# Kernel optimization log

Hardware: AMD Instinct MI355X
Metric: run time of the kernel (lower is better)

The kernel has to match this reference:

```python
import jax, jax.numpy as jnp
import numpy as np

K = 4  # correlation radius -> (2K+1)**2 = 81 displacement channels


def setup_inputs() -> dict:
    key = jax.random.key(0)
    kx, ky = jax.random.split(key)
    x = jax.random.normal(kx, (4, 64, 256, 256), dtype=jnp.float32)
    y = jax.random.normal(ky, (4, 64, 256, 256), dtype=jnp.float32)
    return {"x": x, "y": y}


def reference(x, y):
    b, c, ph, pw = x.shape
    k = K
    # reflect-pad y by k on both spatial dims (matches F.pad(..., 'reflect'))
    yp = jnp.pad(y, ((0, 0), (0, 0), (k, k), (k, k)), mode="reflect")
    # fixed 81-offset loop (trace-time); each term: channel-sum correlation
    outs = [
        jnp.sum(x * jax.lax.dynamic_slice(yp, (0, 0, k + i, k + j), (b, c, ph, pw)), axis=1)
        for i in range(-k, k + 1)
        for j in range(-k, k + 1)
    ]
    return jnp.stack(outs, axis=1)  # [b, (2k+1)^2, ph, pw]
```

## Files before the change

kernel.cpp:

```cpp
#include <hip/hip_runtime.h>


#define HH   256
#define WW   256
#define CCH  64
#define KRAD 4
#define ND   81

#define WT   16
#define HT   16
#define WY   24
#define RSTRIDE 128
#define YRING 10
#define YSLOT (WY * RSTRIDE)
#define PSTRIDE 68

typedef __attribute__((ext_vector_type(8))) short bf16x8;
typedef __attribute__((ext_vector_type(4))) float f32x4;

__device__ __forceinline__ int reflect(int v, int n) {
    v = v < 0 ? -v : v;
    return v >= n ? 2 * n - 2 - v : v;
}
__device__ __forceinline__ unsigned f2bf_pk(float a, float b) {
    union { float f; unsigned u; } xa, xb;
    xa.f = a; xb.f = b;
    unsigned ra = (xa.u + 0x7fffu + ((xa.u >> 16) & 1u)) >> 16;
    unsigned rb = (xb.u + 0x7fffu + ((xb.u >> 16) & 1u)) >> 16;
    return ra | (rb << 16);
}
__device__ __forceinline__ int mod10(int s) {
    if (s >= 20) s -= 20; else if (s >= 10) s -= 10;
    return s;
}

__global__ __launch_bounds__(256, 4) void corr_mfma_kernel(
    const float* __restrict__ x, const float* __restrict__ y,
    float* __restrict__ out)
{
    __shared__ char lds[YRING * YSLOT + ND * PSTRIDE + 12];
    char* ylds   = lds;
    char* pstage = lds + YRING * YSLOT;

    const int d  = blockIdx.x;
    const int v  = (d & 7) * 128 + (d >> 3);
    const int b  = v >> 8;
    const int by = (v >> 4) & 15;
    const int bx = v & 15;
    const int w0 = bx * WT;
    const int h0 = by * HT;

    const int t    = threadIdx.x;
    const int wid  = t >> 6;
    const int lane = t & 63;
    const int lq   = lane >> 4;
    const int ln   = lane & 15;

    const size_t plane = (size_t)HH * WW;
    const float* yb = y + (size_t)b * CCH * plane;
    const float* xb = x + (size_t)b * CCH * plane;

    const int yp  = t & 31;
    const int ycg = t >> 5;

    auto loadY = [&](int hrow, float* v8) {
        int gh = reflect(hrow, HH);
        int pc = yp < WY ? yp : WY - 1;
        int gw = reflect(w0 - KRAD + pc, WW);
        const float* src = yb + (size_t)(ycg * 8) * plane + (size_t)gh * WW + gw;
#pragma unroll
        for (int j = 0; j < 8; ++j) v8[j] = src[(size_t)j * plane];
    };
    auto writeY = [&](int slot, const float* v8) {
        if (yp < WY) {
            char* dst = ylds + slot * YSLOT + yp * RSTRIDE
                      + (((unsigned)(ycg * 16)) ^ ((unsigned)(yp & 7) << 4));
            union { unsigned u[4]; uint4 q; } pk;
#pragma unroll
            for (int m = 0; m < 4; ++m)
                pk.u[m] = f2bf_pk(v8[2 * m], v8[2 * m + 1]);
            *(uint4*)dst = pk.q;
        }
    };
    auto loadX = [&](int hrow, float* v16) {
        int gh = reflect(hrow, HH);
        const float* src = xb + (size_t)(lq * 8) * plane + (size_t)gh * WW + (w0 + ln);
#pragma unroll
        for (int j = 0; j < 8; ++j) v16[j] = src[(size_t)j * plane];
        const float* src2 = src + (size_t)32 * plane;
#pragma unroll
        for (int j = 0; j < 8; ++j) v16[8 + j] = src2[(size_t)j * plane];
    };
    auto xconv = [&](const float* v16, bf16x8& f0, bf16x8& f1) {
        union { unsigned u[4]; bf16x8 v; } c0, c1;
#pragma unroll
        for (int m = 0; m < 4; ++m) {
            c0.u[m] = f2bf_pk(v16[2 * m], v16[2 * m + 1]);
            c1.u[m] = f2bf_pk(v16[8 + 2 * m], v16[9 + 2 * m]);
        }
        f0 = c0.v; f1 = c1.v;
    };

    float yv[8], yv2[8], xv[16];
    bf16x8 bf0, bf1;

    loadY(h0 - KRAD, yv);
    loadX(h0, xv);
#pragma unroll 1
    for (int j = 0; j < 9; ++j) {
        if (j < 8) loadY(h0 - KRAD + j + 1, yv2);
        writeY(j, yv);
#pragma unroll
        for (int m = 0; m < 8; ++m) yv[m] = yv2[m];
    }
    xconv(xv, bf0, bf1);
    __syncthreads();

    const int mbase = lq * 4;
    const int prow  = t >> 4;
    const int pcol  = t & 15;

#pragma unroll 1
    for (int hh = 0; hh < HT; ++hh) {
        const int h = h0 + hh;

        loadY(h + KRAD + 1, yv);
        loadX(h + 1, xv);

        for (int u = wid; u < 18; u += 4) {
            const int di = u >> 1;
            const int wt = u & 1;
            const int slot = mod10(hh + di);
            const char* abase = ylds + slot * YSLOT + (wt * 16 + ln) * RSTRIDE;
            const unsigned sw = (unsigned)(ln & 7) << 4;
            bf16x8 af0 = *(const bf16x8*)(abase + (((unsigned)(lq * 16)) ^ sw));
            bf16x8 af1 = *(const bf16x8*)(abase + (((unsigned)(64 + lq * 16)) ^ sw));
            f32x4 dacc = {0.f, 0.f, 0.f, 0.f};
            dacc = __builtin_amdgcn_mfma_f32_16x16x32_bf16(af0, bf0, dacc, 0, 0, 0);
            dacc = __builtin_amdgcn_mfma_f32_16x16x32_bf16(af1, bf1, dacc, 0, 0, 0);
            char* psu = pstage + di * (9 * PSTRIDE) + ln * 4;
#pragma unroll
            for (int r = 0; r < 4; ++r) {
                const int vr = mbase + r - ln + (wt ? 16 : 0);
                if ((unsigned)vr <= 8u)
                    *(float*)(psu + vr * PSTRIDE) = dacc[r];
            }
        }

        writeY(mod10(hh + 9), yv);
        xconv(xv, bf0, bf1);

        __builtin_amdgcn_sched_barrier(0);
        asm volatile("s_waitcnt lgkmcnt(0)" ::: "memory");
        __builtin_amdgcn_s_barrier();
        __builtin_amdgcn_sched_barrier(0);

        {
            float* og = out + (size_t)b * ND * plane + (size_t)h * WW + (w0 + pcol);
#pragma unroll
            for (int p = 0; p < 6; ++p) {
                const int didx = p * 16 + prow;
                if (p < 5 || prow == 0) {
                    float vv = *(const float*)(pstage + didx * PSTRIDE + pcol * 4);
                    og[(size_t)didx * plane] = vv;
                }
            }
        }

        __builtin_amdgcn_sched_barrier(0);
        __builtin_amdgcn_s_barrier();
        __builtin_amdgcn_sched_barrier(0);
    }
}

extern "C" void kernel_launch(void* const* d_in, const int* in_sizes, int n_in,
                              void* d_out, int out_size, void* d_ws, size_t ws_size,
                              hipStream_t stream) {
    const float* x = (const float*)d_in[0];
    const float* y = (const float*)d_in[1];
    float* out = (float*)d_out;

    dim3 grid(1024);
    dim3 block(256);
    corr_mfma_kernel<<<grid, block, 0, stream>>>(x, y, out);
}
```

Before: 57.59 us.

## Widen tile to 32 columns with 512-thread blocks and per-wave displacement split

Doubles the block tile width from 16 to 32 pixels and the block size to 512 threads, halving the grid. Each wave now owns a fixed 16x16 quadrant and a fixed range of vertical displacements, with the valid-store masks precomputed outside the loop. The wider tile cuts the share of the y halo that is reloaded, since 40 columns are loaded for 32 outputs instead of 24 for 16. In exchange it uses more LDS per block, leaves some threads idle during y loads, and adds an extra LDS wait before the second barrier.

```diff
diff --git a/kernel.cpp b/kernel.cpp
--- a/kernel.cpp
+++ b/kernel.cpp
@@ -7,13 +7,13 @@
 #define KRAD 4
 #define ND   81
 
-#define WT   16
+#define WT   32
 #define HT   16
-#define WY   24
+#define WY   40
 #define RSTRIDE 128
 #define YRING 10
 #define YSLOT (WY * RSTRIDE)
-#define PSTRIDE 68
+#define PSTRIDE 136
 
 typedef __attribute__((ext_vector_type(8))) short bf16x8;
 typedef __attribute__((ext_vector_type(4))) float f32x4;
@@ -34,19 +34,19 @@
     return s;
 }
 
-__global__ __launch_bounds__(256, 4) void corr_mfma_kernel(
+__global__ __launch_bounds__(512, 4) void corr_mfma_kernel(
     const float* __restrict__ x, const float* __restrict__ y,
     float* __restrict__ out)
 {
-    __shared__ char lds[YRING * YSLOT + ND * PSTRIDE + 12];
+    __shared__ char lds[YRING * YSLOT + 1024 + ND * PSTRIDE];
     char* ylds   = lds;
-    char* pstage = lds + YRING * YSLOT;
+    char* pstage = lds + YRING * YSLOT + 1024;
 
     const int d  = blockIdx.x;
-    const int v  = (d & 7) * 128 + (d >> 3);
-    const int b  = v >> 8;
-    const int by = (v >> 4) & 15;
-    const int bx = v & 15;
+    const int v  = (d & 7) * 64 + (d >> 3);
+    const int bx = v & 7;
+    const int by = (v >> 3) & 15;
+    const int b  = v >> 7;
     const int w0 = bx * WT;
     const int h0 = by * HT;
 
@@ -56,25 +56,32 @@
     const int lq   = lane >> 4;
     const int ln   = lane & 15;
 
+    const int p    = wid & 3;
+    const int pm   = (p + 1) >> 1;
+    const int pn   = p >> 1;
+    const int dlo  = (wid >> 2) ? 5 : 0;
+    const int dhi  = (wid >> 2) ? 9 : 5;
+
     const size_t plane = (size_t)HH * WW;
     const float* yb = y + (size_t)b * CCH * plane;
     const float* xb = x + (size_t)b * CCH * plane;
 
-    const int yp  = t & 31;
-    const int ycg = t >> 5;
+    const int yw  = t >> 3;
+    const int ycg = t & 7;
 
-    auto loadY = [&](int hrow, float* v8) {
-        int gh = reflect(hrow, HH);
-        int pc = yp < WY ? yp : WY - 1;
-        int gw = reflect(w0 - KRAD + pc, WW);
-        const float* src = yb + (size_t)(ycg * 8) * plane + (size_t)gh * WW + gw;
+    auto loadY = [&](int L, float* v8) {
+        if (t < 320) {
+            int gh = reflect(h0 - KRAD + L, HH);
+            int gw = reflect(w0 - KRAD + yw, WW);
+            const float* src = yb + (size_t)(ycg * 8) * plane + (size_t)gh * WW + gw;
 #pragma unroll
-        for (int j = 0; j < 8; ++j) v8[j] = src[(size_t)j * plane];
+            for (int j = 0; j < 8; ++j) v8[j] = src[(size_t)j * plane];
+        }
     };
     auto writeY = [&](int slot, const float* v8) {
-        if (yp < WY) {
-            char* dst = ylds + slot * YSLOT + yp * RSTRIDE
-                      + (((unsigned)(ycg * 16)) ^ ((unsigned)(yp & 7) << 4));
+        if (t < 320) {
+            char* dst = ylds + slot * YSLOT + yw * RSTRIDE
+                      + (((unsigned)(ycg * 16)) ^ ((unsigned)(yw & 7) << 4));
             union { unsigned u[4]; uint4 q; } pk;
 #pragma unroll
             for (int m = 0; m < 4; ++m)
@@ -84,7 +91,8 @@
     };
     auto loadX = [&](int hrow, float* v16) {
         int gh = reflect(hrow, HH);
-        const float* src = xb + (size_t)(lq * 8) * plane + (size_t)gh * WW + (w0 + ln);
+        const float* src = xb + (size_t)(lq * 8) * plane + (size_t)gh * WW
+                         + (w0 + pn * 16 + ln);
 #pragma unroll
         for (int j = 0; j < 8; ++j) v16[j] = src[(size_t)j * plane];
         const float* src2 = src + (size_t)32 * plane;
@@ -101,14 +109,24 @@
         f0 = c0.v; f1 = c1.v;
     };
 
+    int vr[4]; bool ok[4];
+#pragma unroll
+    for (int r = 0; r < 4; ++r) {
+        vr[r] = (pm - pn) * 16 + lq * 4 + r - ln;
+        ok[r] = (unsigned)vr[r] <= 8u;
+    }
+
+    const int pcol = t & 31;
+    const int prow = t >> 5;
+
     float yv[8], yv2[8], xv[16];
     bf16x8 bf0, bf1;
 
-    loadY(h0 - KRAD, yv);
+    loadY(0, yv);
     loadX(h0, xv);
 #pragma unroll 1
     for (int j = 0; j < 9; ++j) {
-        if (j < 8) loadY(h0 - KRAD + j + 1, yv2);
+        if (j < 8) loadY(j + 1, yv2);
         writeY(j, yv);
 #pragma unroll
         for (int m = 0; m < 8; ++m) yv[m] = yv2[m];
@@ -116,35 +134,27 @@
     xconv(xv, bf0, bf1);
     __syncthreads();
 
-    const int mbase = lq * 4;
-    const int prow  = t >> 4;
-    const int pcol  = t & 15;
+    const unsigned swl = ((unsigned)(ln & 7)) << 4;
 
 #pragma unroll 1
     for (int hh = 0; hh < HT; ++hh) {
         const int h = h0 + hh;
 
-        loadY(h + KRAD + 1, yv);
+        loadY(hh + 9, yv);
         loadX(h + 1, xv);
 
-        for (int u = wid; u < 18; u += 4) {
-            const int di = u >> 1;
-            const int wt = u & 1;
-            const int slot = mod10(hh + di);
-            const char* abase = ylds + slot * YSLOT + (wt * 16 + ln) * RSTRIDE;
-            const unsigned sw = (unsigned)(ln & 7) << 4;
-            bf16x8 af0 = *(const bf16x8*)(abase + (((unsigned)(lq * 16)) ^ sw));
-            bf16x8 af1 = *(const bf16x8*)(abase + (((unsigned)(64 + lq * 16)) ^ sw));
+        for (int dii = dlo; dii < dhi; ++dii) {
+            const int slot = mod10(hh + dii);
+            const char* arow = ylds + slot * YSLOT + (pm * 16 + ln) * RSTRIDE;
+            bf16x8 af0 = *(const bf16x8*)(arow + (((unsigned)(lq * 16)) ^ swl));
+            bf16x8 af1 = *(const bf16x8*)(arow + (((unsigned)(64 + lq * 16)) ^ swl));
             f32x4 dacc = {0.f, 0.f, 0.f, 0.f};
             dacc = __builtin_amdgcn_mfma_f32_16x16x32_bf16(af0, bf0, dacc, 0, 0, 0);
             dacc = __builtin_amdgcn_mfma_f32_16x16x32_bf16(af1, bf1, dacc, 0, 0, 0);
-            char* psu = pstage + di * (9 * PSTRIDE) + ln * 4;
+            char* psu = pstage + dii * (9 * PSTRIDE) + (pn * 16 + ln) * 4;
 #pragma unroll
-            for (int r = 0; r < 4; ++r) {
-                const int vr = mbase + r - ln + (wt ? 16 : 0);
-                if ((unsigned)vr <= 8u)
-                    *(float*)(psu + vr * PSTRIDE) = dacc[r];
-            }
+            for (int r = 0; r < 4; ++r)
+                if (ok[r]) *(float*)(psu + vr[r] * PSTRIDE) = dacc[r];
         }
 
         writeY(mod10(hh + 9), yv);
@@ -158,16 +168,17 @@
         {
             float* og = out + (size_t)b * ND * plane + (size_t)h * WW + (w0 + pcol);
 #pragma unroll
-            for (int p = 0; p < 6; ++p) {
-                const int didx = p * 16 + prow;
-                if (p < 5 || prow == 0) {
-                    float vv = *(const float*)(pstage + didx * PSTRIDE + pcol * 4);
-                    og[(size_t)didx * plane] = vv;
+            for (int pp = 0; pp < 6; ++pp) {
+                const int row = pp * 16 + prow;
+                if (pp < 5 || prow == 0) {
+                    float vv = *(const float*)(pstage + row * PSTRIDE + pcol * 4);
+                    og[(size_t)row * plane] = vv;
                 }
             }
         }
 
         __builtin_amdgcn_sched_barrier(0);
+        asm volatile("s_waitcnt lgkmcnt(0)" ::: "memory");
         __builtin_amdgcn_s_barrier();
         __builtin_amdgcn_sched_barrier(0);
     }
@@ -180,7 +191,7 @@
     const float* y = (const float*)d_in[1];
     float* out = (float*)d_out;
 
-    dim3 grid(1024);
-    dim3 block(256);
+    dim3 grid(512);
+    dim3 block(512);
     corr_mfma_kernel<<<grid, block, 0, stream>>>(x, y, out);
 }
```

New measurement: 73.83 us. +28.2%, slower.

## Double-buffer output staging to drop second barrier per row

Applied to the files above, without the earlier changes.

The correlation-result staging area in LDS is double-buffered. Each row's outputs are written to global memory at the start of the next iteration, overlapping the MFMA work, which removes one of the two block barriers per row. LDS use grows, so launch bounds drop from 4 to 3 blocks per SM and the staging stride changes from 68 to 72. A final epilogue flushes the last row.

```diff
diff --git a/kernel.cpp b/kernel.cpp
--- a/kernel.cpp
+++ b/kernel.cpp
@@ -13,7 +13,8 @@
 #define RSTRIDE 128
 #define YRING 10
 #define YSLOT (WY * RSTRIDE)
-#define PSTRIDE 68
+#define PSTRIDE 72
+#define PSLOT (ND * PSTRIDE)
 
 typedef __attribute__((ext_vector_type(8))) short bf16x8;
 typedef __attribute__((ext_vector_type(4))) float f32x4;
@@ -34,11 +35,11 @@
     return s;
 }
 
-__global__ __launch_bounds__(256, 4) void corr_mfma_kernel(
+__global__ __launch_bounds__(256, 3) void corr_mfma_kernel(
     const float* __restrict__ x, const float* __restrict__ y,
     float* __restrict__ out)
 {
-    __shared__ char lds[YRING * YSLOT + ND * PSTRIDE + 12];
+    __shared__ char lds[YRING * YSLOT + 2 * PSLOT];
     char* ylds   = lds;
     char* pstage = lds + YRING * YSLOT;
 
@@ -127,6 +128,20 @@
         loadY(h + KRAD + 1, yv);
         loadX(h + 1, xv);
 
+        if (hh > 0) {
+            const char* ps = pstage + ((hh & 1) ^ 1) * PSLOT;
+            float* og = out + (size_t)b * ND * plane + (size_t)(h - 1) * WW + (w0 + pcol);
+#pragma unroll
+            for (int pp = 0; pp < 6; ++pp) {
+                const int row = pp * 16 + prow;
+                if (pp < 5 || prow == 0) {
+                    float vv = *(const float*)(ps + row * PSTRIDE + pcol * 4);
+                    og[(size_t)row * plane] = vv;
+                }
+            }
+        }
+
+        char* pcur = pstage + (hh & 1) * PSLOT;
         for (int u = wid; u < 18; u += 4) {
             const int di = u >> 1;
             const int wt = u & 1;
@@ -138,7 +153,7 @@
             f32x4 dacc = {0.f, 0.f, 0.f, 0.f};
             dacc = __builtin_amdgcn_mfma_f32_16x16x32_bf16(af0, bf0, dacc, 0, 0, 0);
             dacc = __builtin_amdgcn_mfma_f32_16x16x32_bf16(af1, bf1, dacc, 0, 0, 0);
-            char* psu = pstage + di * (9 * PSTRIDE) + ln * 4;
+            char* psu = pcur + di * (9 * PSTRIDE) + ln * 4;
 #pragma unroll
             for (int r = 0; r < 4; ++r) {
                 const int vr = mbase + r - ln + (wt ? 16 : 0);
@@ -154,22 +169,19 @@
         asm volatile("s_waitcnt lgkmcnt(0)" ::: "memory");
         __builtin_amdgcn_s_barrier();
         __builtin_amdgcn_sched_barrier(0);
+    }
 
-        {
-            float* og = out + (size_t)b * ND * plane + (size_t)h * WW + (w0 + pcol);
+    {
+        const char* ps = pstage + ((HT - 1) & 1) * PSLOT;
+        float* og = out + (size_t)b * ND * plane + (size_t)(h0 + HT - 1) * WW + (w0 + pcol);
 #pragma unroll
-            for (int p = 0; p < 6; ++p) {
-                const int didx = p * 16 + prow;
-                if (p < 5 || prow == 0) {
-                    float vv = *(const float*)(pstage + didx * PSTRIDE + pcol * 4);
-                    og[(size_t)didx * plane] = vv;
-                }
+        for (int pp = 0; pp < 6; ++pp) {
+            const int row = pp * 16 + prow;
+            if (pp < 5 || prow == 0) {
+                float vv = *(const float*)(ps + row * PSTRIDE + pcol * 4);
+                og[(size_t)row * plane] = vv;
             }
         }
-
-        __builtin_amdgcn_sched_barrier(0);
-        __builtin_amdgcn_s_barrier();
-        __builtin_amdgcn_sched_barrier(0);
     }
 }
 
```

New measurement: 68.84 us. +19.5%, slower.
